# Performance work log

Hardware: AMD Instinct MI355X
Metric: run time of the kernel (lower is better)

## Reference

```python
import jax, jax.numpy as jnp
import numpy as np

B, S, D, H, DFF = 2, 2048, 1024, 16, 4096
DH = D // H
EPS = 1e-5


def setup_inputs() -> dict:
    key = jax.random.key(0)
    ks = jax.random.split(key, 12)
    s = 0.02
    x = jax.random.normal(ks[0], (B, S, D), dtype=jnp.float32)
    # causal decoder mask, True = keep
    mask = jnp.tril(jnp.ones((S, S), dtype=bool))[None, None, :, :]
    Wq = jax.random.normal(ks[1], (D, D), dtype=jnp.float32) * s
    Wk = jax.random.normal(ks[2], (D, D), dtype=jnp.float32) * s
    Wv = jax.random.normal(ks[3], (D, D), dtype=jnp.float32) * s
    Wo = jax.random.normal(ks[4], (D, D), dtype=jnp.float32) * s
    w1 = jax.random.normal(ks[5], (D, DFF), dtype=jnp.float32) * s
    b1 = jnp.zeros((DFF,), dtype=jnp.float32)
    w2 = jax.random.normal(ks[6], (DFF, D), dtype=jnp.float32) * s
    b2 = jnp.zeros((D,), dtype=jnp.float32)
    g1 = jnp.ones((D,), dtype=jnp.float32)
    be1 = jnp.zeros((D,), dtype=jnp.float32)
    g2 = jnp.ones((D,), dtype=jnp.float32)
    be2 = jnp.zeros((D,), dtype=jnp.float32)
    return dict(x=x, mask=mask, Wq=Wq, Wk=Wk, Wv=Wv, Wo=Wo,
                w1=w1, b1=b1, w2=w2, b2=b2, g1=g1, be1=be1, g2=g2, be2=be2)


def _layer_norm(x, gamma, beta):
    mu = jnp.mean(x, axis=-1, keepdims=True)
    var = jnp.mean(jnp.square(x - mu), axis=-1, keepdims=True)
    return (x - mu) * jax.lax.rsqrt(var + EPS) * gamma + beta


def _attention(x, mask, Wq, Wk, Wv, Wo):
    # x: [B,S,D] -> q,k,v: [B,H,S,DH]
    def split_heads(t):
        return t.reshape(x.shape[0], x.shape[1], H, DH).transpose(0, 2, 1, 3)
    q = split_heads(x @ Wq)
    k = split_heads(x @ Wk)
    v = split_heads(x @ Wv)
    scores = jnp.einsum('bhqd,bhkd->bhqk', q, k) / jnp.sqrt(jnp.float32(DH))
    scores = jnp.where(mask, scores, jnp.float32(-1e9))
    probs = jax.nn.softmax(scores, axis=-1)
    out = jnp.einsum('bhqk,bhkd->bhqd', probs, v)  # [B,H,S,DH]
    out = out.transpose(0, 2, 1, 3).reshape(x.shape[0], x.shape[1], -1)
    return out @ Wo


def reference(x, mask, Wq, Wk, Wv, Wo, w1, b1, w2, b2, g1, be1, g2, be2):
    # residual 1: pre-norm self-attention (dropout=0)
    h = x + _attention(_layer_norm(x, g1, be1), mask, Wq, Wk, Wv, Wo)
    # residual 2: pre-norm FFN
    hn = _layer_norm(h, g2, be2)
    ffn = jax.nn.relu(hn @ w1 + b1) @ w2 + b2
    return h + ffn
```

## Files before the change

kernel.cpp:

```cpp
#include <hip/hip_runtime.h>

typedef unsigned short u16;
typedef __attribute__((ext_vector_type(8))) short short8;
typedef __attribute__((ext_vector_type(4))) float f32x4;

#define CB 2
#define CS 2048
#define CD 1024
#define CH 16
#define CDH 64
#define CDFF 4096
#define NQB (CS / 64)

__device__ __forceinline__ u16 f2bf(float f){
  union { float f; unsigned u; } x; x.f = f;
  unsigned r = (x.u + 0x7fffu + ((x.u >> 16) & 1u)) >> 16;
  return (u16)r;
}

__device__ __forceinline__ u16 f2bf_pos(float f){
  union { float f; unsigned u; } x; x.f = f;
  return (u16)((x.u + 0x8000u) >> 16);
}

__device__ __forceinline__ void gload_lds16(const void* g, void* l){
  __builtin_amdgcn_global_load_lds(
    (const __attribute__((address_space(1))) void*)(unsigned long long)g,
    (__attribute__((address_space(3))) void*)(unsigned long long)l,
    16, 0, 0);
}


struct TPAll { const float* s[6]; u16* d[6]; };

__global__ __launch_bounds__(256)
void prep_all(TPAll p, const float* __restrict__ x, const float* __restrict__ g1,
              const float* __restrict__ be1, u16* __restrict__ yln)
{
  const int g = blockIdx.x >> 12;
  const int id = blockIdx.x & 4095;
  const int tid = threadIdx.x;

  if (g == 3){
    const int row = id;
    const int lane = tid & 63, wave = tid >> 6;
    const float4 v = ((const float4*)(x + (size_t)row * CD))[tid];
    float s  = v.x + v.y + v.z + v.w;
    float s2 = v.x*v.x + v.y*v.y + v.z*v.z + v.w*v.w;
    #pragma unroll
    for (int m = 1; m < 64; m <<= 1){ s += __shfl_xor(s, m); s2 += __shfl_xor(s2, m); }
    __shared__ float red[8];
    if (lane == 0){ red[wave] = s; red[4 + wave] = s2; }
    __syncthreads();
    s  = red[0] + red[1] + red[2] + red[3];
    s2 = red[4] + red[5] + red[6] + red[7];
    const float mu = s * (1.0f / CD);
    const float var = s2 * (1.0f / CD) - mu * mu;
    const float rs = rsqrtf(var + 1e-5f);
    const float4 gv = ((const float4*)g1)[tid];
    const float4 bv = ((const float4*)be1)[tid];
    ushort4 o;
    o.x = f2bf((v.x - mu) * rs * gv.x + bv.x);
    o.y = f2bf((v.y - mu) * rs * gv.y + bv.y);
    o.z = f2bf((v.z - mu) * rs * gv.z + bv.z);
    o.w = f2bf((v.w - mu) * rs * gv.w + bv.w);
    ((ushort4*)yln)[(size_t)row * (CD / 4) + tid] = o;
    return;
  }

  __shared__ float t[32][33];
  const float* __restrict__ in;
  u16* __restrict__ out;
  int K, N, n0, k0;
  if (g == 0){
    const int w = id >> 10, tile = id & 1023;
    in = p.s[w]; out = p.d[w]; K = 1024; N = 1024;
    n0 = (tile & 31) * 32; k0 = (tile >> 5) * 32;
  } else if (g == 1){
    in = p.s[4]; out = p.d[4]; K = 1024; N = 4096;
    n0 = (id & 127) * 32; k0 = (id >> 7) * 32;
  } else {
    in = p.s[5]; out = p.d[5]; K = 4096; N = 1024;
    n0 = (id & 31) * 32; k0 = (id >> 5) * 32;
  }
  const int c = tid & 31, r4 = tid >> 5;
  #pragma unroll
  for (int i = 0; i < 4; i++){
    int r = r4 + i * 8;
    t[r][c] = in[(size_t)(k0 + r) * N + n0 + c];
  }
  __syncthreads();
  #pragma unroll
  for (int i = 0; i < 4; i++){
    int r = r4 + i * 8;
    out[(size_t)(n0 + r) * K + k0 + c] = f2bf(t[c][r]);
  }
}

template<int MODE>
__global__ __launch_bounds__(256)
void ln_bf16(const float* __restrict__ xin, const float* __restrict__ g,
             const float* __restrict__ be, u16* __restrict__ outp,
             float4* __restrict__ aux, const float* __restrict__ bias)
{
  const int row = blockIdx.x, tid = threadIdx.x;
  const int lane = tid & 63, wave = tid >> 6;
  const float4 v = ((const float4*)(xin + (size_t)row * CD))[tid];
  float s  = v.x + v.y + v.z + v.w;
  float s2 = v.x*v.x + v.y*v.y + v.z*v.z + v.w*v.w;
  #pragma unroll
  for (int m = 1; m < 64; m <<= 1){ s += __shfl_xor(s, m); s2 += __shfl_xor(s2, m); }
  __shared__ float red[8];
  if (lane == 0){ red[wave] = s; red[4 + wave] = s2; }

  if (MODE == 2){
    const float4 b4 = ((const float4*)bias)[tid];
    float4 w = v;
    w.x += b4.x; w.y += b4.y; w.z += b4.z; w.w += b4.w;
    aux[(size_t)row * 256 + tid] = w;
  }

  __syncthreads();
  s  = red[0] + red[1] + red[2] + red[3];
  s2 = red[4] + red[5] + red[6] + red[7];
  const float mu = s * (1.0f / CD);
  const float var = s2 * (1.0f / CD) - mu * mu;
  const float rs = rsqrtf(var + 1e-5f);
  const float4 gv = ((const float4*)g)[tid];
  const float4 bv = ((const float4*)be)[tid];
  ushort4 o;
  o.x = f2bf((v.x - mu) * rs * gv.x + bv.x);
  o.y = f2bf((v.y - mu) * rs * gv.y + bv.y);
  o.z = f2bf((v.z - mu) * rs * gv.z + bv.z);
  o.w = f2bf((v.w - mu) * rs * gv.w + bv.w);
  ((ushort4*)outp)[(size_t)row * (CD / 4) + tid] = o;
}

template<int EPI>
__global__ __launch_bounds__(512)
void gemm_bt(const u16* __restrict__ A, const u16* __restrict__ Bt,
             void* __restrict__ Cout, const float* __restrict__ bias,
             int M, int N, int K,
             int ldc, int vsplit, u16* __restrict__ vtout)
{
  __shared__ __align__(16) u16 sA[2][2][128 * 64];
  __shared__ __align__(16) u16 sB[2][2][128 * 64];
  const int tid = threadIdx.x;
  const int wave = tid >> 6, lane = tid & 63;
  const int wm = wave >> 2, wn = wave & 3;

  const int G = gridDim.x;
  const int flat = blockIdx.x;
  const int t0_ = (flat & 7) * (G >> 3) + (flat >> 3);
  const int NN = N >> 8;
  const int n_i = t0_ % NN;
  const int m_i = t0_ / NN;

  const int m0 = m_i * 256, n0 = n_i * 256;
  const int lq = lane >> 4, lr = lane & 15;
  const int l7 = lr & 7;
  const int sw0 = ((lq ^ l7) << 3);
  const int sw1 = (((4 + lq) ^ l7) << 3);

  f32x4 acc[8][4] = {};

  const u16* Ab = A + (size_t)m0 * K;
  const u16* Bb = Bt + (size_t)n0 * K;
  const int srow = lane >> 3;
  const int scol = (((lane & 7) ^ srow)) * 8;

  auto stageA = [&](int par, int h, int kt){
    const u16* src = Ab + (size_t)(h * 128) * K + kt * 64;
    u16* dst = &sA[par][h][0];
    #pragma unroll
    for (int i = 0; i < 2; i++){
      const int c = wave * 2 + i;
      gload_lds16(src + (size_t)(c * 8 + srow) * K + scol, dst + c * 512);
    }
  };
  auto stageB = [&](int par, int h, int kt){
    const u16* src = Bb + (size_t)(h * 128) * K + kt * 64;
    u16* dst = &sB[par][h][0];
    #pragma unroll
    for (int i = 0; i < 2; i++){
      const int c = wave * 2 + i;
      gload_lds16(src + (size_t)(c * 8 + srow) * K + scol, dst + c * 512);
    }
  };

  const int nt = K >> 6;

  stageB(0, 0, 0); stageB(0, 1, 0);
  stageA(0, 0, 0); stageA(0, 1, 0);
  stageB(1, 0, 1); stageB(1, 1, 1);
  asm volatile("s_waitcnt vmcnt(4)\n\ts_barrier" ::: "memory");

  short8 bF0[4], bF1[4];

  for (int t = 0; t < nt; t++){
    const int par = t & 1;
    const u16* aT = &sA[par][wm][0];
    const u16* bT = &sB[par][wn >> 1][0];
    const int bbase = (wn & 1) * 64;

    #pragma unroll
    for (int tq = 0; tq < 4; tq++){
      if (tq == 0){
        #pragma unroll
        for (int j = 0; j < 4; j++){
          bF0[j] = *(const short8*)&bT[(bbase + j * 16 + lr) * 64 + sw0];
          bF1[j] = *(const short8*)&bT[(bbase + j * 16 + lr) * 64 + sw1];
        }
      }
      const short8 a00 = *(const short8*)&aT[((tq * 2 + 0) * 16 + lr) * 64 + sw0];
      const short8 a01 = *(const short8*)&aT[((tq * 2 + 0) * 16 + lr) * 64 + sw1];
      const short8 a10 = *(const short8*)&aT[((tq * 2 + 1) * 16 + lr) * 64 + sw0];
      const short8 a11 = *(const short8*)&aT[((tq * 2 + 1) * 16 + lr) * 64 + sw1];

      if (tq == 0){ if (t + 1 < nt) stageA(par ^ 1, 0, t + 1); }
      if (tq == 1){ if (t + 1 < nt) stageA(par ^ 1, 1, t + 1); }
      if (tq == 2){ if (t + 2 < nt) stageB(par, 0, t + 2); }
      if (tq == 3){ if (t + 2 < nt) stageB(par, 1, t + 2); }

      asm volatile("s_barrier" ::: "memory");
      asm volatile("s_waitcnt lgkmcnt(0)" ::: "memory");
      __builtin_amdgcn_sched_barrier(0);

      __builtin_amdgcn_s_setprio(1);
      #pragma unroll
      for (int j = 0; j < 4; j++){
        acc[tq * 2 + 0][j] = __builtin_amdgcn_mfma_f32_16x16x32_bf16(a00, bF0[j], acc[tq * 2 + 0][j], 0, 0, 0);
        acc[tq * 2 + 0][j] = __builtin_amdgcn_mfma_f32_16x16x32_bf16(a01, bF1[j], acc[tq * 2 + 0][j], 0, 0, 0);
        acc[tq * 2 + 1][j] = __builtin_amdgcn_mfma_f32_16x16x32_bf16(a10, bF0[j], acc[tq * 2 + 1][j], 0, 0, 0);
        acc[tq * 2 + 1][j] = __builtin_amdgcn_mfma_f32_16x16x32_bf16(a11, bF1[j], acc[tq * 2 + 1][j], 0, 0, 0);
      }
      __builtin_amdgcn_s_setprio(0);

      if (tq == 3){
        if (t == nt - 2){
          asm volatile("s_waitcnt vmcnt(0)\n\ts_barrier" ::: "memory");
        } else if (t < nt - 2){
          asm volatile("s_waitcnt vmcnt(4)\n\ts_barrier" ::: "memory");
        } else {
          asm volatile("s_barrier" ::: "memory");
        }
      } else {
        asm volatile("s_barrier" ::: "memory");
      }
    }
  }

  if (EPI == 0 && n0 >= vsplit){
    #pragma unroll
    for (int mf = 0; mf < 8; mf++){
      const int row0 = m0 + wm * 128 + mf * 16 + lq * 4;
      const int bb = row0 >> 11, s = row0 & 2047;
      #pragma unroll
      for (int nf = 0; nf < 4; nf++){
        const int col = n0 - vsplit + wn * 64 + nf * 16 + lr;
        ushort4 o;
        o.x = f2bf(acc[mf][nf][0]); o.y = f2bf(acc[mf][nf][1]);
        o.z = f2bf(acc[mf][nf][2]); o.w = f2bf(acc[mf][nf][3]);
        *(ushort4*)&vtout[((size_t)(bb * 1024 + col)) * CS + s] = o;
      }
    }
    return;
  }

  const float osc = (EPI == 0 && n0 < 1024) ? 0.125f : 1.0f;

  #pragma unroll
  for (int mf = 0; mf < 8; mf++){
    const int row = m0 + wm * 128 + mf * 16 + lq * 4;
    #pragma unroll
    for (int nf = 0; nf < 4; nf++){
      const int col = n0 + wn * 64 + nf * 16 + lr;
      #pragma unroll
      for (int r = 0; r < 4; r++){
        float v = acc[mf][nf][r];
        const size_t off = (size_t)(row + r) * ldc + col;
        if (EPI == 0){
          ((u16*)Cout)[off] = f2bf(v * osc);
        } else {
          v += bias[col]; v = v > 0.0f ? v : 0.0f;
          ((u16*)Cout)[off] = f2bf(v);
        }
      }
    }
  }
}

__global__ __launch_bounds__(256)
void gemm_bt64(const u16* __restrict__ A, const u16* __restrict__ Bt,
               const float* __restrict__ resid, float* __restrict__ Cout,
               int M, int N, int K)
{
  __shared__ __align__(16) u16 lA[3][64 * 64];
  __shared__ __align__(16) u16 lB[3][128 * 64];
  const int tid = threadIdx.x;
  const int wave = tid >> 6, lane = tid & 63;

  const int G = gridDim.x;
  const int flat = blockIdx.x;
  const int t = (flat & 7) * (G >> 3) + (flat >> 3);
  const int NN = N >> 7;
  const int n_i = t % NN;
  const int m_i = t / NN;
  const int m0 = m_i * 64, n0 = n_i * 128;
  const int lq = lane >> 4, lr = lane & 15;
  const int l7 = lr & 7;
  const int sw0 = ((lq ^ l7) << 3);
  const int sw1 = (((4 + lq) ^ l7) << 3);

  f32x4 acc[4][2] = {};

  const u16* Ab = A + (size_t)m0 * K;
  const u16* Bb = Bt + (size_t)n0 * K;
  const int srow = lane >> 3;
  const int scol = (((lane & 7) ^ srow)) * 8;

  auto stage = [&](int buf, int kt){
    const int k0 = kt * 64;
    #pragma unroll
    for (int i = 0; i < 6; i++){
      const int c = i * 4 + wave;
      if (c < 8){
        gload_lds16(Ab + (size_t)(c * 8 + srow) * K + k0 + scol, &lA[buf][c * 512]);
      } else {
        const int cb2 = c - 8;
        gload_lds16(Bb + (size_t)(cb2 * 8 + srow) * K + k0 + scol, &lB[buf][cb2 * 512]);
      }
    }
  };

  const int nit = K >> 6;
  stage(0, 0);
  stage(1, 1);
  int cb = 0;
  for (int i = 0; i < nit; i++){
    if (i + 2 < nit){
      stage((cb + 2 >= 3) ? cb - 1 : cb + 2, i + 2);
      asm volatile("s_waitcnt vmcnt(12)\n\ts_barrier" ::: "memory");
    } else if (i + 1 < nit){
      asm volatile("s_waitcnt vmcnt(6)\n\ts_barrier" ::: "memory");
    } else {
      asm volatile("s_waitcnt vmcnt(0)\n\ts_barrier" ::: "memory");
    }
    #pragma unroll
    for (int kh = 0; kh < 2; kh++){
      const int sw = kh ? sw1 : sw0;
      short8 aF[4], bF[2];
      #pragma unroll
      for (int i2 = 0; i2 < 4; i2++) aF[i2] = *(const short8*)&lA[cb][(i2 * 16 + lr) * 64 + sw];
      #pragma unroll
      for (int j = 0; j < 2; j++) bF[j] = *(const short8*)&lB[cb][(wave * 32 + j * 16 + lr) * 64 + sw];
      #pragma unroll
      for (int i2 = 0; i2 < 4; i2++)
        #pragma unroll
        for (int j = 0; j < 2; j++)
          acc[i2][j] = __builtin_amdgcn_mfma_f32_16x16x32_bf16(aF[i2], bF[j], acc[i2][j], 0, 0, 0);
    }
    asm volatile("s_barrier" ::: "memory");
    cb = (cb + 1 >= 3) ? 0 : cb + 1;
  }

  #pragma unroll
  for (int i = 0; i < 4; i++){
    const int row = m0 + i * 16 + lq * 4;
    #pragma unroll
    for (int j = 0; j < 2; j++){
      const int col = n0 + wave * 32 + j * 16 + lr;
      #pragma unroll
      for (int r = 0; r < 4; r++){
        const size_t off = (size_t)(row + r) * N + col;
        Cout[off] = resid[off] + acc[i][j][r];
      }
    }
  }
}

__global__ __launch_bounds__(256)
void attn_kernel(const u16* __restrict__ qk, const u16* __restrict__ vt,
                 u16* __restrict__ outp)
{
  __shared__ __align__(16) u16 lK[2][64 * 64];
  __shared__ __align__(16) u16 lVt[2][64 * 64];
  __shared__ __align__(16) u16 lP[4][16 * 72];
  const int tid = threadIdx.x, wave = tid >> 6, lane = tid & 63;
  const int lq = lane >> 4, lr = lane & 15;
  const int l7 = lr & 7;
  const int sw0 = ((lq ^ l7) << 3);
  const int sw1 = (((4 + lq) ^ l7) << 3);
  const int bh = blockIdx.x, b = bh >> 4, h = bh & 15;
  const int RS = 2048;
  const int srow = lane >> 3;
  const int scol = (((lane & 7) ^ srow)) * 8;

  const size_t kbase = (size_t)(b * CS) * RS + 1024 + h * CDH;
  const size_t vbase = (size_t)(bh * CDH) * CS;
  u16* lPw = lP[wave];

  auto stageKV = [&](int buf, int kt){
    #pragma unroll
    for (int cc = 0; cc < 2; cc++){
      const int c = wave * 2 + cc;
      gload_lds16(qk + kbase + (size_t)(kt * 64 + c * 8 + srow) * RS + scol, &lK[buf][c * 512]);
      gload_lds16(vt + vbase + (size_t)(c * 8 + srow) * CS + kt * 64 + scol, &lVt[buf][c * 512]);
    }
  };

  const int iq = (NQB - 1) - blockIdx.y;
  const int q0 = iq * 64;
  const int ktmax = iq + 1;

  const int qrow = b * CS + q0 + wave * 16 + lr;
  const u16* qp = qk + (size_t)qrow * RS + h * CDH;
  const short8 qf0 = *(const short8*)(qp + lq * 8);
  const short8 qf1 = *(const short8*)(qp + 32 + lq * 8);

  f32x4 o[4] = {};
  float lsum = 0.0f;
  const int qg = q0 + wave * 16 + lr;

  stageKV(0, 0);
  for (int kt = 0; kt < ktmax; ++kt){
    const int cb = kt & 1;
    if (kt + 1 < ktmax){
      stageKV(cb ^ 1, kt + 1);
      asm volatile("s_waitcnt vmcnt(4)\n\ts_barrier" ::: "memory");
    } else {
      asm volatile("s_waitcnt vmcnt(0)\n\ts_barrier" ::: "memory");
    }

    f32x4 s[4] = {};
    #pragma unroll
    for (int nb = 0; nb < 4; nb++){
      const short8 bk0 = *(const short8*)&lK[cb][(nb * 16 + lr) * 64 + sw0];
      const short8 bk1 = *(const short8*)&lK[cb][(nb * 16 + lr) * 64 + sw1];
      s[nb] = __builtin_amdgcn_mfma_f32_16x16x32_bf16(bk0, qf0, s[nb], 0, 0, 0);
      s[nb] = __builtin_amdgcn_mfma_f32_16x16x32_bf16(bk1, qf1, s[nb], 0, 0, 0);
    }

    const bool diag = (kt + 1) == ktmax;
    #pragma unroll
    for (int nb = 0; nb < 4; nb++){
      float e0 = __expf(s[nb][0]);
      float e1 = __expf(s[nb][1]);
      float e2 = __expf(s[nb][2]);
      float e3 = __expf(s[nb][3]);
      if (diag){
        const int kb = kt * 64 + nb * 16 + lq * 4;
        e0 = (kb     <= qg) ? e0 : 0.0f;
        e1 = (kb + 1 <= qg) ? e1 : 0.0f;
        e2 = (kb + 2 <= qg) ? e2 : 0.0f;
        e3 = (kb + 3 <= qg) ? e3 : 0.0f;
      }
      lsum += (e0 + e1) + (e2 + e3);
      ushort4 pw;
      pw.x = f2bf_pos(e0);
      pw.y = f2bf_pos(e1);
      pw.z = f2bf_pos(e2);
      pw.w = f2bf_pos(e3);
      *(ushort4*)&lPw[lr * 72 + nb * 16 + lq * 4] = pw;
    }

    asm volatile("s_waitcnt lgkmcnt(0)" ::: "memory");
    const short8 pf0 = *(const short8*)&lPw[lr * 72 + lq * 8];
    const short8 pf1 = *(const short8*)&lPw[lr * 72 + 32 + lq * 8];

    #pragma unroll
    for (int nb = 0; nb < 4; nb++){
      const short8 bv0 = *(const short8*)&lVt[cb][(nb * 16 + lr) * 64 + sw0];
      const short8 bv1 = *(const short8*)&lVt[cb][(nb * 16 + lr) * 64 + sw1];
      o[nb] = __builtin_amdgcn_mfma_f32_16x16x32_bf16(pf0, bv0, o[nb], 0, 0, 0);
      o[nb] = __builtin_amdgcn_mfma_f32_16x16x32_bf16(pf1, bv1, o[nb], 0, 0, 0);
    }
    asm volatile("s_barrier" ::: "memory");
  }

  float l = lsum;
  l += __shfl_xor(l, 16);
  l += __shfl_xor(l, 32);
  const float inv = __builtin_amdgcn_rcpf(l);

  #pragma unroll
  for (int r = 0; r < 4; r++){
    const float invr = __shfl(inv, lq * 4 + r);
    const size_t row = (size_t)(b * CS + q0 + wave * 16 + lq * 4 + r);
    #pragma unroll
    for (int nb = 0; nb < 4; nb++)
      outp[row * CD + h * CDH + nb * 16 + lr] = f2bf(o[nb][r] * invr);
  }
}

extern "C" void kernel_launch(void* const* d_in, const int* in_sizes, int n_in,
                              void* d_out, int out_size, void* d_ws, size_t ws_size,
                              hipStream_t stream)
{
  const float* x   = (const float*)d_in[0];
  const float* Wq  = (const float*)d_in[2];
  const float* Wk  = (const float*)d_in[3];
  const float* Wv  = (const float*)d_in[4];
  const float* Wo  = (const float*)d_in[5];
  const float* w1  = (const float*)d_in[6];
  const float* b1  = (const float*)d_in[7];
  const float* w2  = (const float*)d_in[8];
  const float* b2  = (const float*)d_in[9];
  const float* g1  = (const float*)d_in[10];
  const float* be1 = (const float*)d_in[11];
  const float* g2  = (const float*)d_in[12];
  const float* be2 = (const float*)d_in[13];
  float* out = (float*)d_out;

  char* ws = (char*)d_ws;
  const size_t MB = 1u << 20;
  u16* yln    = (u16*)(ws);
  u16* qk     = (u16*)(ws + 8  * MB);
  u16* vt     = (u16*)(ws + 24 * MB);
  u16* attn   = (u16*)(ws + 32 * MB);
  u16* mid    = (u16*)(ws + 40 * MB);
  u16* Wqkv_t = (u16*)(ws + 72 * MB);
  u16* Wo_t   = (u16*)(ws + 78 * MB);
  u16* w1_t   = (u16*)(ws + 80 * MB);
  u16* w2_t   = (u16*)(ws + 88 * MB);

  const int M = CB * CS;
  const int BIG = 1 << 30;

  TPAll pa;
  pa.s[0] = Wq; pa.s[1] = Wk; pa.s[2] = Wv; pa.s[3] = Wo; pa.s[4] = w1; pa.s[5] = w2;
  pa.d[0] = Wqkv_t;
  pa.d[1] = Wqkv_t + (size_t)CD * CD;
  pa.d[2] = Wqkv_t + (size_t)2 * CD * CD;
  pa.d[3] = Wo_t;
  pa.d[4] = w1_t;
  pa.d[5] = w2_t;
  prep_all<<<4 * 4096, 256, 0, stream>>>(pa, x, g1, be1, yln);

  gemm_bt<0><<<192, 512, 0, stream>>>(yln, Wqkv_t, qk, nullptr, M, 3 * CD, CD, 2048, 2048, vt);
  attn_kernel<<<dim3(CB * CH, NQB), 256, 0, stream>>>(qk, vt, attn);
  gemm_bt64<<<64 * 8, 256, 0, stream>>>(attn, Wo_t, x, out, M, CD, CD);
  ln_bf16<2><<<M, 256, 0, stream>>>(out, g2, be2, yln, (float4*)out, b2);
  gemm_bt<1><<<256, 512, 0, stream>>>(yln, w1_t, mid, b1, M, CDFF, CD, CDFF, BIG, nullptr);
  gemm_bt64<<<64 * 8, 256, 0, stream>>>(mid, w2_t, out, out, M, CD, CDFF);
}
```

Baseline: 315.1 us.

## Split K across wave pairs in gemm_bt64 and load A directly into registers

Restructures the residual GEMM so the four waves form a 2x2 grid over N and K halves. Each wave computes a 64x64 partial result over its half of each K tile, and the two K halves are reduced through LDS at the end. The A operand is no longer staged in LDS: it is loaded straight from global memory into registers one iteration ahead, and the vmcnt waits are retuned to match. This aims to cut LDS traffic and raise the MFMA-to-LDS-read ratio. In exchange it adds an LDS reduction epilogue, more accumulator registers, and uncoalesced per-lane global loads for A.

Result: slower. 410.9 us (+30.4%).

```diff
diff --git a/kernel.cpp b/kernel.cpp
--- a/kernel.cpp
+++ b/kernel.cpp
@@ -295,7 +295,6 @@
                const float* __restrict__ resid, float* __restrict__ Cout,
                int M, int N, int K)
 {
-  __shared__ __align__(16) u16 lA[3][64 * 64];
   __shared__ __align__(16) u16 lB[3][128 * 64];
   const int tid = threadIdx.x;
   const int wave = tid >> 6, lane = tid & 63;
@@ -309,71 +308,108 @@
   const int m0 = m_i * 64, n0 = n_i * 128;
   const int lq = lane >> 4, lr = lane & 15;
   const int l7 = lr & 7;
-  const int sw0 = ((lq ^ l7) << 3);
-  const int sw1 = (((4 + lq) ^ l7) << 3);
-
-  f32x4 acc[4][2] = {};
+  const int wn2 = wave & 1, wk = wave >> 1;
+  const int swK = ((wk * 4 + lq) ^ l7) << 3;
+
+  f32x4 acc[4][4] = {};
 
   const u16* Ab = A + (size_t)m0 * K;
   const u16* Bb = Bt + (size_t)n0 * K;
   const int srow = lane >> 3;
   const int scol = (((lane & 7) ^ srow)) * 8;
 
-  auto stage = [&](int buf, int kt){
+  auto stageB = [&](int buf, int kt){
     const int k0 = kt * 64;
     #pragma unroll
-    for (int i = 0; i < 6; i++){
-      const int c = i * 4 + wave;
-      if (c < 8){
-        gload_lds16(Ab + (size_t)(c * 8 + srow) * K + k0 + scol, &lA[buf][c * 512]);
-      } else {
-        const int cb2 = c - 8;
-        gload_lds16(Bb + (size_t)(cb2 * 8 + srow) * K + k0 + scol, &lB[buf][cb2 * 512]);
-      }
+    for (int ii = 0; ii < 4; ii++){
+      const int c = ii * 4 + wave;
+      gload_lds16(Bb + (size_t)(c * 8 + srow) * K + k0 + scol, &lB[buf][c * 512]);
     }
   };
+  auto loadA = [&](short8* a, int kt){
+    const u16* ap = Ab + (size_t)lr * K + kt * 64 + wk * 32 + lq * 8;
+    #pragma unroll
+    for (int i2 = 0; i2 < 4; i2++)
+      a[i2] = *(const short8*)(ap + (size_t)(i2 * 16) * K);
+  };
 
   const int nit = K >> 6;
-  stage(0, 0);
-  stage(1, 1);
-  int cb = 0;
-  for (int i = 0; i < nit; i++){
-    if (i + 2 < nit){
-      stage((cb + 2 >= 3) ? cb - 1 : cb + 2, i + 2);
+
+  auto kstep = [&](int i, short8* aC, short8* aN){
+    const int cb = i % 3;
+    if (i + 2 < nit) stageB((i + 2) % 3, i + 2);
+    if (i + 1 < nit) loadA(aN, i + 1);
+    if (i == 0){
       asm volatile("s_waitcnt vmcnt(12)\n\ts_barrier" ::: "memory");
+    } else if (i == 1){
+      asm volatile("s_waitcnt vmcnt(16)\n\ts_barrier" ::: "memory");
+    } else if (i + 2 < nit){
+      asm volatile("s_waitcnt vmcnt(20)\n\ts_barrier" ::: "memory");
     } else if (i + 1 < nit){
-      asm volatile("s_waitcnt vmcnt(6)\n\ts_barrier" ::: "memory");
+      asm volatile("s_waitcnt vmcnt(16)\n\ts_barrier" ::: "memory");
     } else {
-      asm volatile("s_waitcnt vmcnt(0)\n\ts_barrier" ::: "memory");
-    }
-    #pragma unroll
-    for (int kh = 0; kh < 2; kh++){
-      const int sw = kh ? sw1 : sw0;
-      short8 aF[4], bF[2];
-      #pragma unroll
-      for (int i2 = 0; i2 < 4; i2++) aF[i2] = *(const short8*)&lA[cb][(i2 * 16 + lr) * 64 + sw];
-      #pragma unroll
-      for (int j = 0; j < 2; j++) bF[j] = *(const short8*)&lB[cb][(wave * 32 + j * 16 + lr) * 64 + sw];
-      #pragma unroll
-      for (int i2 = 0; i2 < 4; i2++)
+      asm volatile("s_waitcnt vmcnt(8)\n\ts_barrier" ::: "memory");
+    }
+    short8 bF[4];
+    #pragma unroll
+    for (int j = 0; j < 4; j++)
+      bF[j] = *(const short8*)&lB[cb][(wn2 * 64 + j * 16 + lr) * 64 + swK];
+    #pragma unroll
+    for (int i2 = 0; i2 < 4; i2++)
+      #pragma unroll
+      for (int j = 0; j < 4; j++)
+        acc[i2][j] = __builtin_amdgcn_mfma_f32_16x16x32_bf16(aC[i2], bF[j], acc[i2][j], 0, 0, 0);
+    asm volatile("s_barrier" ::: "memory");
+  };
+
+  short8 aA[4], aB[4];
+  loadA(aA, 0);
+  stageB(0, 0);
+  stageB(1, 1);
+
+  kstep(0, aA, aB);
+  kstep(1, aB, aA);
+  for (int i = 2; i < nit; i += 2){
+    kstep(i,     aA, aB);
+    kstep(i + 1, aB, aA);
+  }
+
+  float* xch = (float*)&lB[0][0];
+  {
+    const int give0 = wk ? 0 : 2;
+    const int halfw = wk ? 0 : 1;
+    #pragma unroll
+    for (int i2l = 0; i2l < 2; i2l++)
+      #pragma unroll
+      for (int j = 0; j < 4; j++)
+        *(f32x4*)&xch[(((wn2 * 2 + halfw) * 8) + i2l * 4 + j) * 256 + lane * 4] = acc[give0 + i2l][j];
+  }
+  __syncthreads();
+  {
+    const int keep0 = wk ? 2 : 0;
+    const int halfr = wk ? 1 : 0;
+    #pragma unroll
+    for (int i2l = 0; i2l < 2; i2l++){
+      const int i2 = keep0 + i2l;
+      #pragma unroll
+      for (int j = 0; j < 4; j++){
+        const f32x4 p = *(const f32x4*)&xch[(((wn2 * 2 + halfr) * 8) + i2l * 4 + j) * 256 + lane * 4];
+        acc[i2][j][0] += p[0]; acc[i2][j][1] += p[1];
+        acc[i2][j][2] += p[2]; acc[i2][j][3] += p[3];
+      }
+    }
+    #pragma unroll
+    for (int i2l = 0; i2l < 2; i2l++){
+      const int i2 = keep0 + i2l;
+      const int row = m0 + i2 * 16 + lq * 4;
+      #pragma unroll
+      for (int j = 0; j < 4; j++){
+        const int col = n0 + wn2 * 64 + j * 16 + lr;
         #pragma unroll
-        for (int j = 0; j < 2; j++)
-          acc[i2][j] = __builtin_amdgcn_mfma_f32_16x16x32_bf16(aF[i2], bF[j], acc[i2][j], 0, 0, 0);
-    }
-    asm volatile("s_barrier" ::: "memory");
-    cb = (cb + 1 >= 3) ? 0 : cb + 1;
-  }
-
-  #pragma unroll
-  for (int i = 0; i < 4; i++){
-    const int row = m0 + i * 16 + lq * 4;
-    #pragma unroll
-    for (int j = 0; j < 2; j++){
-      const int col = n0 + wave * 32 + j * 16 + lr;
-      #pragma unroll
-      for (int r = 0; r < 4; r++){
-        const size_t off = (size_t)(row + r) * N + col;
-        Cout[off] = resid[off] + acc[i][j][r];
+        for (int r = 0; r < 4; r++){
+          const size_t off = (size_t)(row + r) * N + col;
+          Cout[off] = resid[off] + acc[i2][j][r];
+        }
       }
     }
   }
```
